# Optimization experiments

Hardware: AMD Instinct MI355X
Metric: run time of the kernel (lower is better)

The kernel has to match this reference:

```python
import jax, jax.numpy as jnp
import numpy as np

ALPHA = 0.5
BETA = 5.0
LOGIT_SCALE = 100.0  # exp(log(100)) -- CLIP's learned logit scale at its clamp value
NUM_CLASSES = 200


def _l2norm(x):
    return x / jnp.linalg.norm(x, axis=-1, keepdims=True)


def setup_inputs() -> dict:
    key = jax.random.key(0)
    k1, k2, k3, k4 = jax.random.split(key, 4)
    img_f = jax.random.normal(k1, (1024, 512), dtype=jnp.float32)
    text_features = jax.random.normal(k2, (200, 512), dtype=jnp.float32)
    keys = jax.random.normal(k3, (50000, 512), dtype=jnp.float32)
    labels = jax.random.randint(k4, (50000,), 0, NUM_CLASSES, dtype=jnp.int64)
    return {"img_f": img_f, "text_features": text_features, "keys": keys, "labels": labels}


def reference(img_f, text_features, keys, labels):
    # encode_image output is L2-normalized in the module; keys were built from
    # normalized image features, text_features are normalized class embeddings.
    q = _l2norm(img_f)            # [B, D]
    t = _l2norm(text_features)    # [C, D]
    k = _l2norm(keys)             # [N, D]

    # CLIP zero-shot branch: scale * q @ t.T -> [B, C]
    z = LOGIT_SCALE * jnp.einsum('bd,cd->bc', q, t)

    # Tip-Adapter cache branch: exp(beta * q @ keys.T) @ one_hot(labels)
    sim = jnp.einsum('bd,nd->bn', q, k)                 # [B, N]
    aff = jnp.exp(BETA * sim)                           # [B, N]
    values = jax.nn.one_hot(labels, NUM_CLASSES, dtype=aff.dtype)  # [N, C]
    c = aff @ values                                    # [B, C]

    return (1.0 - ALPHA) * z + ALPHA * c
```

## Files before the change

### kernel.cpp

```cpp
#include <hip/hip_runtime.h>

#define B_Q    1024
#define D_K    512
#define N_CLS  200
#define N_KEYS 50000
#define N_PAD  50048
#define N_ZT   (N_PAD / 128)
#define NT_TOT (N_ZT + 2)
#define KN_ROWS 50304
#define HS     16

#define R0 N_PAD
#define R1 (R0 + B_Q)
#define R2 (R1 + N_CLS)
#define R3 (R2 + 56)
#define R4 (R3 + 400)

typedef __attribute__((ext_vector_type(8))) short bf16x8;
typedef __attribute__((ext_vector_type(4))) float f32x4;

__device__ __forceinline__ unsigned short f2bf(float f) {
  union { float f; unsigned int i; } v; v.f = f;
  unsigned int r = v.i + 0x7fffu + ((v.i >> 16) & 1u);
  return (unsigned short)(r >> 16);
}
__device__ __forceinline__ uint4 pack8(const float f[8], float s) {
  uint4 o;
  o.x = (unsigned)f2bf(f[0]*s) | ((unsigned)f2bf(f[1]*s) << 16);
  o.y = (unsigned)f2bf(f[2]*s) | ((unsigned)f2bf(f[3]*s) << 16);
  o.z = (unsigned)f2bf(f[4]*s) | ((unsigned)f2bf(f[5]*s) << 16);
  o.w = (unsigned)f2bf(f[6]*s) | ((unsigned)f2bf(f[7]*s) << 16);
  return o;
}
__device__ __forceinline__ void async_copy16(const void* g, void* lds) {
  __builtin_amdgcn_global_load_lds(
      (const __attribute__((address_space(1))) unsigned int*)g,
      (__attribute__((address_space(3))) unsigned int*)lds, 16, 0, 0);
}

__global__ void k_zero(int* __restrict__ g) {
  int i = blockIdx.x * 1024 + threadIdx.x;
  if (i < 2 * N_CLS * HS) g[i] = 0;
}

__global__ __launch_bounds__(256) void k_rank(const int* __restrict__ labels,
                                              const int* __restrict__ ghist,
                                              int* __restrict__ gcnt,
                                              int* __restrict__ perm,
                                              int* __restrict__ cls) {
  __shared__ int incl[N_CLS];
  __shared__ int histl[N_CLS];
  int t = threadIdx.x;
  if (t < N_CLS) { int h = ghist[t * HS]; histl[t] = h; incl[t] = h; }
  __syncthreads();
  for (int d = 1; d < N_CLS; d <<= 1) {
    int x = 0;
    if (t < N_CLS && t >= d) x = incl[t - d];
    __syncthreads();
    if (t < N_CLS) incl[t] += x;
    __syncthreads();
  }
  int n = blockIdx.x * 256 + t;
  if (n < N_KEYS) {
    int lab = labels[n];
    int r = atomicAdd(&gcnt[lab * HS], 1);
    int d = incl[lab] - histl[lab] + r;
    perm[d] = n;
    cls[d] = lab;
  } else if (n < KN_ROWS) {
    perm[n] = n;
    cls[n] = N_CLS;
  }
}

__global__ void k_prep2(const float* __restrict__ keys, const float* __restrict__ img,
                        const float* __restrict__ txt, const int* __restrict__ labels,
                        unsigned short* __restrict__ qn, unsigned short* __restrict__ kn,
                        int* __restrict__ ghist, float* __restrict__ out) {
  int w = threadIdx.x >> 6, lane = threadIdx.x & 63;
  int row = blockIdx.x * 4 + w;
  const float* src; unsigned short* dst;
  if (row < R0) {
    if (row >= N_KEYS) {
      *((uint4*)(kn + (size_t)row * D_K) + lane) = make_uint4(0, 0, 0, 0);
      return;
    }
    if (lane == 0) atomicAdd(&ghist[labels[row] * HS], 1);
    src = keys + (size_t)row * D_K;
    dst = kn + (size_t)row * D_K;
  } else if (row < R1) {
    int r = row - R0;
    src = img + (size_t)r * D_K;
    dst = qn + (size_t)r * D_K;
  } else if (row < R2) {
    int r = row - R1;
    src = txt + (size_t)r * D_K;
    dst = kn + (size_t)(N_PAD + r) * D_K;
  } else if (row < R3) {
    int r = N_PAD + N_CLS + (row - R2);
    *((uint4*)(kn + (size_t)r * D_K) + lane) = make_uint4(0, 0, 0, 0);
    return;
  } else if (row < R4) {
    int zr = row - R3;
    uint4* o4 = (uint4*)(out + (size_t)zr * 512) + lane * 2;
    o4[0] = make_uint4(0, 0, 0, 0);
    o4[1] = make_uint4(0, 0, 0, 0);
    return;
  } else return;
  const float4* s4 = (const float4*)src + lane * 2;
  float4 a = s4[0], b = s4[1];
  float f[8] = {a.x, a.y, a.z, a.w, b.x, b.y, b.z, b.w};
  float ss = 0.f;
#pragma unroll
  for (int i = 0; i < 8; i++) ss += f[i] * f[i];
#pragma unroll
  for (int d = 1; d < 64; d <<= 1) ss += __shfl_xor(ss, d);
  float rinv = rsqrtf(ss);
  *((uint4*)dst + lane) = pack8(f, rinv);
}

__global__ __launch_bounds__(256, 3) void k_main(const unsigned short* __restrict__ qn,
                                                 const unsigned short* __restrict__ kn,
                                                 const int* __restrict__ cls,
                                                 const int* __restrict__ perm,
                                                 float* __restrict__ out) {
  __shared__ unsigned short As[128 * 64];
  __shared__ unsigned short Bs[128 * 64];
  int t = threadIdx.x;
  int wsw = (blockIdx.x & 7) * NT_TOT + (blockIdx.x >> 3);
  int tileN = wsw >> 3, tileB = wsw & 7;
  int rowB0 = tileB * 128, rowN0 = tileN * 128;

  f32x4 acc[4][4];
#pragma unroll
  for (int i = 0; i < 4; i++)
#pragma unroll
    for (int j = 0; j < 4; j++) acc[i][j] = (f32x4){0.f, 0.f, 0.f, 0.f};

  int lane = t & 63, w = t >> 6;
  int wr = (w >> 1) * 64, wc = (w & 1) * 64;
  int l15 = lane & 15, lq = lane >> 4;
  const int rA = t >> 3;
  const int gsw = ((t & 7) ^ (rA & 7)) * 8;
  const int sw = l15 & 7;

  int prow[4];
#pragma unroll
  for (int i = 0; i < 4; i++) prow[i] = perm[rowN0 + i * 32 + rA];
  int cj[4];
#pragma unroll
  for (int j = 0; j < 4; j++) cj[j] = cls[rowN0 + wc + 16 * j + l15];
  int cseg0 = cls[rowN0 + wc];
  int cseg1 = cls[rowN0 + wc + 63];

  for (int k0 = 0; k0 < D_K; k0 += 64) {
    __syncthreads();
#pragma unroll
    for (int i = 0; i < 4; i++) {
      int row = i * 32 + rA;
      async_copy16(qn + (size_t)(rowB0 + row) * D_K + k0 + gsw, &As[i * 2048 + t * 8]);
      async_copy16(kn + (size_t)prow[i] * D_K + k0 + gsw, &Bs[i * 2048 + t * 8]);
    }
    __syncthreads();
#pragma unroll
    for (int ks = 0; ks < 64; ks += 32) {
      bf16x8 af[4], bf[4];
#pragma unroll
      for (int i = 0; i < 4; i++)
        af[i] = *(const bf16x8*)&As[(wr + 16 * i + l15) * 64 + ((((ks >> 3) + lq) ^ sw) * 8)];
#pragma unroll
      for (int j = 0; j < 4; j++)
        bf[j] = *(const bf16x8*)&Bs[(wc + 16 * j + l15) * 64 + ((((ks >> 3) + lq) ^ sw) * 8)];
#pragma unroll
      for (int i = 0; i < 4; i++)
#pragma unroll
        for (int j = 0; j < 4; j++)
          acc[i][j] = __builtin_amdgcn_mfma_f32_16x16x32_bf16(af[i], bf[j], acc[i][j], 0, 0, 0);
    }
  }

  if (tileN >= N_ZT) {
#pragma unroll
    for (int i = 0; i < 4; i++)
#pragma unroll
      for (int j = 0; j < 4; j++) {
        int col = rowN0 + wc + 16 * j + l15 - N_PAD;
        if (col < N_CLS) {
#pragma unroll
          for (int r = 0; r < 4; r++) {
            int row = rowB0 + wr + 16 * i + lq * 4 + r;
            atomicAdd(out + (size_t)row * N_CLS + col, 50.0f * acc[i][j][r]);
          }
        }
      }
    return;
  }

#pragma unroll
  for (int i = 0; i < 4; i++)
#pragma unroll
    for (int j = 0; j < 4; j++)
#pragma unroll
      for (int r = 0; r < 4; r++) acc[i][j][r] = __expf(5.0f * acc[i][j][r]);

  for (int c = cseg0; c <= cseg1; c++) {
    if (c >= N_CLS) break;
#pragma unroll
    for (int i = 0; i < 4; i++) {
      float s0 = 0.f, s1 = 0.f, s2 = 0.f, s3 = 0.f;
#pragma unroll
      for (int j = 0; j < 4; j++) {
        if (cj[j] == c) {
          s0 += acc[i][j][0]; s1 += acc[i][j][1];
          s2 += acc[i][j][2]; s3 += acc[i][j][3];
        }
      }
#pragma unroll
      for (int d = 1; d < 16; d <<= 1) {
        s0 += __shfl_xor(s0, d); s1 += __shfl_xor(s1, d);
        s2 += __shfl_xor(s2, d); s3 += __shfl_xor(s3, d);
      }
      if (l15 == 0) {
        int row = rowB0 + wr + 16 * i + lq * 4;
        float* o = out + (size_t)row * N_CLS + c;
        if (s0 != 0.f) atomicAdd(o + 0 * N_CLS, 0.5f * s0);
        if (s1 != 0.f) atomicAdd(o + 1 * N_CLS, 0.5f * s1);
        if (s2 != 0.f) atomicAdd(o + 2 * N_CLS, 0.5f * s2);
        if (s3 != 0.f) atomicAdd(o + 3 * N_CLS, 0.5f * s3);
      }
    }
  }
}

extern "C" void kernel_launch(void* const* d_in, const int* in_sizes, int n_in,
                              void* d_out, int out_size, void* d_ws, size_t ws_size,
                              hipStream_t stream) {
  (void)in_sizes; (void)n_in; (void)out_size; (void)ws_size;
  const float* img    = (const float*)d_in[0];
  const float* txt    = (const float*)d_in[1];
  const float* keys   = (const float*)d_in[2];
  const int*   labels = (const int*)d_in[3];
  float*       out    = (float*)d_out;

  char* ws = (char*)d_ws;
  unsigned short* qn = (unsigned short*)(ws + 0);
  unsigned short* kn = (unsigned short*)(ws + 1048576);
  int*  perm = (int*)(ws + 52559872);
  int*  cls  = (int*)(ws + 52761088);
  int*  gz   = (int*)(ws + 52962304);

  k_zero<<<7, 1024, 0, stream>>>(gz);
  k_prep2<<<(R4 + 3) / 4, 256, 0, stream>>>(keys, img, txt, labels, qn, kn, gz, out);
  k_rank<<<(KN_ROWS + 255) / 256, 256, 0, stream>>>(labels, gz, gz + N_CLS * HS, perm, cls);
  k_main<<<dim3(8 * NT_TOT), 256, 0, stream>>>(qn, kn, cls, perm, out);
}
```

Measured before the change: 253.9 us.

## Double-buffer k_main LDS tiles and aggregate rank atomics per block

The GEMM main loop now uses two LDS buffers, so the async global-to-LDS copy for the next K slice is issued before computing on the current one, with one barrier per iteration. The occupancy hint drops from 3 to 2 blocks per CU to fit the doubled shared memory. k_rank now runs 1024-thread blocks and builds a per-block label histogram in shared memory, so it issues one global atomic per class per block instead of one per key. The trade-offs are lower occupancy in k_main and an extra barrier phase in k_rank.

```diff
diff --git a/kernel.cpp b/kernel.cpp
--- a/kernel.cpp
+++ b/kernel.cpp
@@ -43,15 +43,21 @@
   if (i < 2 * N_CLS * HS) g[i] = 0;
 }
 
-__global__ __launch_bounds__(256) void k_rank(const int* __restrict__ labels,
-                                              const int* __restrict__ ghist,
-                                              int* __restrict__ gcnt,
-                                              int* __restrict__ perm,
-                                              int* __restrict__ cls) {
+__global__ __launch_bounds__(1024) void k_rank(const int* __restrict__ labels,
+                                               const int* __restrict__ ghist,
+                                               int* __restrict__ gcnt,
+                                               int* __restrict__ perm,
+                                               int* __restrict__ cls) {
   __shared__ int incl[N_CLS];
   __shared__ int histl[N_CLS];
+  __shared__ int lhist[N_CLS];
+  __shared__ int lbase[N_CLS];
+  __shared__ int lcur[N_CLS];
   int t = threadIdx.x;
-  if (t < N_CLS) { int h = ghist[t * HS]; histl[t] = h; incl[t] = h; }
+  if (t < N_CLS) {
+    int h = ghist[t * HS];
+    histl[t] = h; incl[t] = h; lhist[t] = 0;
+  }
   __syncthreads();
   for (int d = 1; d < N_CLS; d <<= 1) {
     int x = 0;
@@ -60,11 +66,21 @@
     if (t < N_CLS) incl[t] += x;
     __syncthreads();
   }
-  int n = blockIdx.x * 256 + t;
+  int n = blockIdx.x * 1024 + t;
+  int lab = -1;
   if (n < N_KEYS) {
-    int lab = labels[n];
-    int r = atomicAdd(&gcnt[lab * HS], 1);
-    int d = incl[lab] - histl[lab] + r;
+    lab = labels[n];
+    atomicAdd(&lhist[lab], 1);
+  }
+  __syncthreads();
+  if (t < N_CLS && lhist[t] > 0) {
+    lbase[t] = (incl[t] - histl[t]) + atomicAdd(&gcnt[t * HS], lhist[t]);
+    lcur[t] = 0;
+  }
+  __syncthreads();
+  if (n < N_KEYS) {
+    int r = atomicAdd(&lcur[lab], 1);
+    int d = lbase[lab] + r;
     perm[d] = n;
     cls[d] = lab;
   } else if (n < KN_ROWS) {
@@ -119,13 +135,13 @@
   *((uint4*)dst + lane) = pack8(f, rinv);
 }
 
-__global__ __launch_bounds__(256, 3) void k_main(const unsigned short* __restrict__ qn,
+__global__ __launch_bounds__(256, 2) void k_main(const unsigned short* __restrict__ qn,
                                                  const unsigned short* __restrict__ kn,
                                                  const int* __restrict__ cls,
                                                  const int* __restrict__ perm,
                                                  float* __restrict__ out) {
-  __shared__ unsigned short As[128 * 64];
-  __shared__ unsigned short Bs[128 * 64];
+  __shared__ unsigned short As[2][128 * 64];
+  __shared__ unsigned short Bs[2][128 * 64];
   int t = threadIdx.x;
   int wsw = (blockIdx.x & 7) * NT_TOT + (blockIdx.x >> 3);
   int tileN = wsw >> 3, tileB = wsw & 7;
@@ -153,31 +169,43 @@
   int cseg0 = cls[rowN0 + wc];
   int cseg1 = cls[rowN0 + wc + 63];
 
-  for (int k0 = 0; k0 < D_K; k0 += 64) {
-    __syncthreads();
+  auto stage = [&](int p, int k0) {
 #pragma unroll
     for (int i = 0; i < 4; i++) {
       int row = i * 32 + rA;
-      async_copy16(qn + (size_t)(rowB0 + row) * D_K + k0 + gsw, &As[i * 2048 + t * 8]);
-      async_copy16(kn + (size_t)prow[i] * D_K + k0 + gsw, &Bs[i * 2048 + t * 8]);
-    }
-    __syncthreads();
+      async_copy16(qn + (size_t)(rowB0 + row) * D_K + k0 + gsw, &As[p][i * 2048 + t * 8]);
+      async_copy16(kn + (size_t)prow[i] * D_K + k0 + gsw, &Bs[p][i * 2048 + t * 8]);
+    }
+  };
+  auto compute = [&](int p) {
 #pragma unroll
     for (int ks = 0; ks < 64; ks += 32) {
       bf16x8 af[4], bf[4];
 #pragma unroll
       for (int i = 0; i < 4; i++)
-        af[i] = *(const bf16x8*)&As[(wr + 16 * i + l15) * 64 + ((((ks >> 3) + lq) ^ sw) * 8)];
+        af[i] = *(const bf16x8*)&As[p][(wr + 16 * i + l15) * 64 + ((((ks >> 3) + lq) ^ sw) * 8)];
 #pragma unroll
       for (int j = 0; j < 4; j++)
-        bf[j] = *(const bf16x8*)&Bs[(wc + 16 * j + l15) * 64 + ((((ks >> 3) + lq) ^ sw) * 8)];
+        bf[j] = *(const bf16x8*)&Bs[p][(wc + 16 * j + l15) * 64 + ((((ks >> 3) + lq) ^ sw) * 8)];
 #pragma unroll
       for (int i = 0; i < 4; i++)
 #pragma unroll
         for (int j = 0; j < 4; j++)
           acc[i][j] = __builtin_amdgcn_mfma_f32_16x16x32_bf16(af[i], bf[j], acc[i][j], 0, 0, 0);
     }
-  }
+  };
+
+  stage(0, 0);
+  __syncthreads();
+  int p = 0;
+#pragma unroll
+  for (int k0 = 64; k0 < D_K; k0 += 64) {
+    stage(p ^ 1, k0);
+    compute(p);
+    __syncthreads();
+    p ^= 1;
+  }
+  compute(p);
 
   if (tileN >= N_ZT) {
 #pragma unroll
@@ -251,6 +279,6 @@
 
   k_zero<<<7, 1024, 0, stream>>>(gz);
   k_prep2<<<(R4 + 3) / 4, 256, 0, stream>>>(keys, img, txt, labels, qn, kn, gz, out);
-  k_rank<<<(KN_ROWS + 255) / 256, 256, 0, stream>>>(labels, gz, gz + N_CLS * HS, perm, cls);
+  k_rank<<<(KN_ROWS + 1023) / 1024, 1024, 0, stream>>>(labels, gz, gz + N_CLS * HS, perm, cls);
   k_main<<<dim3(8 * NT_TOT), 256, 0, stream>>>(qn, kn, cls, perm, out);
 }
```

Result: slower. 266.8 us (+5.1%).

## Compute label histogram per block in LDS, dropping zero kernel and global atomics

Applied to the files above, without the earlier changes.

Removes the separate zeroing kernel and the global histogram atomics done in the prep kernel. Each rank block now scans all 50000 labels itself, building a full histogram and a count of labels before its own range in shared memory, then assigns slots with local atomics. This cuts one kernel launch and the global atomic contention, at the cost of every one of the ~50 blocks re-reading the whole label array. The within-class order changes, but the per-class sums are unaffected.

```diff
diff --git a/kernel.cpp b/kernel.cpp
--- a/kernel.cpp
+++ b/kernel.cpp
@@ -8,7 +8,6 @@
 #define N_ZT   (N_PAD / 128)
 #define NT_TOT (N_ZT + 2)
 #define KN_ROWS 50304
-#define HS     16
 
 #define R0 N_PAD
 #define R1 (R0 + B_Q)
@@ -38,20 +37,24 @@
       (__attribute__((address_space(3))) unsigned int*)lds, 16, 0, 0);
 }
 
-__global__ void k_zero(int* __restrict__ g) {
-  int i = blockIdx.x * 1024 + threadIdx.x;
-  if (i < 2 * N_CLS * HS) g[i] = 0;
-}
-
-__global__ __launch_bounds__(256) void k_rank(const int* __restrict__ labels,
-                                              const int* __restrict__ ghist,
-                                              int* __restrict__ gcnt,
-                                              int* __restrict__ perm,
-                                              int* __restrict__ cls) {
+__global__ __launch_bounds__(1024) void k_rank(const int* __restrict__ labels,
+                                               int* __restrict__ perm,
+                                               int* __restrict__ cls) {
+  __shared__ int hall[N_CLS];
+  __shared__ int hbef[N_CLS];
   __shared__ int incl[N_CLS];
-  __shared__ int histl[N_CLS];
+  __shared__ int lcur[N_CLS];
   int t = threadIdx.x;
-  if (t < N_CLS) { int h = ghist[t * HS]; histl[t] = h; incl[t] = h; }
+  int base = blockIdx.x * 1024;
+  if (t < N_CLS) { hall[t] = 0; hbef[t] = 0; lcur[t] = 0; }
+  __syncthreads();
+  for (int idx = t; idx < N_KEYS; idx += 1024) {
+    int lab = labels[idx];
+    atomicAdd(&hall[lab], 1);
+    if (idx < base) atomicAdd(&hbef[lab], 1);
+  }
+  __syncthreads();
+  if (t < N_CLS) incl[t] = hall[t];
   __syncthreads();
   for (int d = 1; d < N_CLS; d <<= 1) {
     int x = 0;
@@ -60,11 +63,11 @@
     if (t < N_CLS) incl[t] += x;
     __syncthreads();
   }
-  int n = blockIdx.x * 256 + t;
+  int n = base + t;
   if (n < N_KEYS) {
     int lab = labels[n];
-    int r = atomicAdd(&gcnt[lab * HS], 1);
-    int d = incl[lab] - histl[lab] + r;
+    int r = atomicAdd(&lcur[lab], 1);
+    int d = (incl[lab] - hall[lab]) + hbef[lab] + r;
     perm[d] = n;
     cls[d] = lab;
   } else if (n < KN_ROWS) {
@@ -74,9 +77,9 @@
 }
 
 __global__ void k_prep2(const float* __restrict__ keys, const float* __restrict__ img,
-                        const float* __restrict__ txt, const int* __restrict__ labels,
+                        const float* __restrict__ txt,
                         unsigned short* __restrict__ qn, unsigned short* __restrict__ kn,
-                        int* __restrict__ ghist, float* __restrict__ out) {
+                        float* __restrict__ out) {
   int w = threadIdx.x >> 6, lane = threadIdx.x & 63;
   int row = blockIdx.x * 4 + w;
   const float* src; unsigned short* dst;
@@ -85,7 +88,6 @@
       *((uint4*)(kn + (size_t)row * D_K) + lane) = make_uint4(0, 0, 0, 0);
       return;
     }
-    if (lane == 0) atomicAdd(&ghist[labels[row] * HS], 1);
     src = keys + (size_t)row * D_K;
     dst = kn + (size_t)row * D_K;
   } else if (row < R1) {
@@ -247,10 +249,8 @@
   unsigned short* kn = (unsigned short*)(ws + 1048576);
   int*  perm = (int*)(ws + 52559872);
   int*  cls  = (int*)(ws + 52761088);
-  int*  gz   = (int*)(ws + 52962304);
-
-  k_zero<<<7, 1024, 0, stream>>>(gz);
-  k_prep2<<<(R4 + 3) / 4, 256, 0, stream>>>(keys, img, txt, labels, qn, kn, gz, out);
-  k_rank<<<(KN_ROWS + 255) / 256, 256, 0, stream>>>(labels, gz, gz + N_CLS * HS, perm, cls);
+
+  k_rank<<<(KN_ROWS + 1023) / 1024, 1024, 0, stream>>>(labels, perm, cls);
+  k_prep2<<<(R4 + 3) / 4, 256, 0, stream>>>(keys, img, txt, qn, kn, out);
   k_main<<<dim3(8 * NT_TOT), 256, 0, stream>>>(qn, kn, cls, perm, out);
 }
```

After: 267.9 us. 1.06x slower.
